# Kernel optimization log

Measured on AMD Instinct MI355X. Metric: run time of the kernel, lower is better.

Reference implementation:

```python
import jax, jax.numpy as jnp
import numpy as np

N = 100_000      # nodes
E = 1_600_000    # edges (avg degree 16)
D_IN, D_HID, D_OUT = 128, 64, 64
NEG_SLOPE = 0.2  # PyG GATConv default


def setup_inputs() -> dict:
    key = jax.random.key(0)
    ks = jax.random.split(key, 10)
    s = lambda k, shape: jax.random.normal(k, shape, jnp.float32) * 0.1
    return {
        "x": jax.random.normal(ks[0], (N, D_IN), jnp.float32),
        "edge_index": jax.random.randint(ks[1], (2, E), 0, N, dtype=jnp.int32),
        "W1": s(ks[2], (D_IN, D_HID)),
        "a_src1": s(ks[3], (D_HID,)),
        "a_dst1": s(ks[4], (D_HID,)),
        "b1": jnp.zeros((D_HID,), jnp.float32),
        "W2": s(ks[5], (D_HID, D_OUT)),
        "a_src2": s(ks[6], (D_OUT,)),
        "a_dst2": s(ks[7], (D_OUT,)),
        "b2": jnp.zeros((D_OUT,), jnp.float32),
    }


def gat_conv(x, src, dst, W, a_src, a_dst, b):
    """Single-head PyG-style GATConv (self-loops already appended to src/dst)."""
    n = x.shape[0]
    h = x @ W                                   # [N, D]
    # per-edge attention logits: leaky_relu(a_src . h_j + a_dst . h_i)
    logit = jax.nn.leaky_relu((h @ a_src)[src] + (h @ a_dst)[dst], NEG_SLOPE)
    # segment softmax over incoming edges of each dst node
    m = jax.ops.segment_max(logit, dst, num_segments=n)
    e = jnp.exp(logit - m[dst])
    denom = jax.ops.segment_sum(e, dst, num_segments=n)
    alpha = e / (denom[dst] + 1e-16)            # [E]
    out = jax.ops.segment_sum(alpha[:, None] * h[src], dst, num_segments=n)
    return out + b


def reference(x, edge_index, W1, a_src1, a_dst1, b1, W2, a_src2, a_dst2, b2):
    n = x.shape[0]
    loops = jnp.arange(n, dtype=edge_index.dtype)  # add_self_loops=True default
    src = jnp.concatenate([edge_index[0], loops])
    dst = jnp.concatenate([edge_index[1], loops])
    h = gat_conv(x, src, dst, W1, a_src1, a_dst1, b1)
    embedding = jax.nn.relu(h)   # dropout = identity (inference semantics)
    out = gat_conv(embedding, src, dst, W2, a_src2, a_dst2, b2)
    return (embedding, out)
```

## Files before the change

### kernel.cpp

```cpp
#include <hip/hip_runtime.h>
#include <hip/hip_bf16.h>

#define DHID 64
#define SUBSH 9
#define SUBSZ (1 << SUBSH)
#define PCAP 16384
#define EB 4096
typedef __attribute__((ext_vector_type(8))) short short8;
typedef __attribute__((ext_vector_type(4))) float f32x4;

static __device__ __forceinline__ short tobf(float f) {
  __hip_bfloat16 h = __float2bfloat16(f);
  return *reinterpret_cast<short*>(&h);
}

__global__ void k_bucket(const int* __restrict__ src, const int* __restrict__ dst,
                         int* __restrict__ bkt, int* __restrict__ bcnt,
                         int E, int nsb, int cap) {
  __shared__ int lcnt[256];
  __shared__ int lbase[256];
  int tid = threadIdx.x;
  int c0 = blockIdx.x * EB;
  if (c0 >= E) return;
  for (int i = tid; i < nsb; i += 256) lcnt[i] = 0;
  __syncthreads();
  int wloc[16], uloc[16];
  #pragma unroll
  for (int k = 0; k < 16; k++) {
    int i = c0 + tid + k * 256;
    if (i < E) {
      int d = dst[i];
      int w = d >> SUBSH;
      wloc[k] = w;
      uloc[k] = (src[i] << SUBSH) | (d & (SUBSZ - 1));
      atomicAdd(&lcnt[w], 1);
    } else wloc[k] = -1;
  }
  __syncthreads();
  for (int i = tid; i < nsb; i += 256) lbase[i] = atomicAdd(&bcnt[i], lcnt[i]);
  __syncthreads();
  for (int i = tid; i < nsb; i += 256) lcnt[i] = 0;
  __syncthreads();
  #pragma unroll
  for (int k = 0; k < 16; k++) {
    int w = wloc[k];
    if (w >= 0) {
      int r = atomicAdd(&lcnt[w], 1);
      bkt[(size_t)w * cap + lbase[w] + r] = uloc[k];
    }
  }
}

__global__ void k_count(const int* __restrict__ bkt, const int* __restrict__ bcnt,
                        int* __restrict__ roff, int N, int cap) {
  __shared__ int h[SUBSZ];
  int sb = blockIdx.x, tid = threadIdx.x;
  for (int j = tid; j < SUBSZ; j += 256) h[j] = 1;
  __syncthreads();
  int n = bcnt[sb];
  const int* b = bkt + (size_t)sb * cap;
  for (int i = tid; i < n; i += 256) atomicAdd(&h[b[i] & (SUBSZ - 1)], 1);
  __syncthreads();
  int d0 = sb << SUBSH, d1 = min(N, d0 + SUBSZ);
  for (int j = tid; j < d1 - d0; j += 256) roff[d0 + j] = h[j];
}

__global__ void k_scan_block(int* __restrict__ buf, int n, int* __restrict__ bsum) {
  __shared__ int lds[256];
  int tid = threadIdx.x;
  int base = blockIdx.x * 1024 + tid * 4;
  int a0 = (base + 0) < n ? buf[base + 0] : 0;
  int a1 = (base + 1) < n ? buf[base + 1] : 0;
  int a2 = (base + 2) < n ? buf[base + 2] : 0;
  int a3 = (base + 3) < n ? buf[base + 3] : 0;
  int s = a0 + a1 + a2 + a3;
  lds[tid] = s; __syncthreads();
  for (int off = 1; off < 256; off <<= 1) {
    int t = (tid >= off) ? lds[tid - off] : 0;
    __syncthreads();
    lds[tid] += t;
    __syncthreads();
  }
  int excl = lds[tid] - s;
  if ((base + 0) < n) buf[base + 0] = excl; excl += a0;
  if ((base + 1) < n) buf[base + 1] = excl; excl += a1;
  if ((base + 2) < n) buf[base + 2] = excl; excl += a2;
  if ((base + 3) < n) buf[base + 3] = excl;
  if (tid == 255) bsum[blockIdx.x] = lds[255];
}

__global__ void k_scan_mid(int* __restrict__ bsum, int nb) {
  int lane = threadIdx.x;
  int v0 = (lane < nb) ? bsum[lane] : 0;
  #pragma unroll
  for (int off = 1; off < 64; off <<= 1) { int t = __shfl_up(v0, off, 64); if (lane >= off) v0 += t; }
  int v1 = (64 + lane) < nb ? bsum[64 + lane] : 0;
  #pragma unroll
  for (int off = 1; off < 64; off <<= 1) { int t = __shfl_up(v1, off, 64); if (lane >= off) v1 += t; }
  v1 += __shfl(v0, 63, 64);
  if (lane < nb) bsum[lane] = v0;
  if ((64 + lane) < nb) bsum[64 + lane] = v1;
}

__global__ void k_scan_add(int* __restrict__ buf, int n, const int* __restrict__ bsum, int nb) {
  int i = blockIdx.x * blockDim.x + threadIdx.x;
  if (i < n) { int c = i >> 10; if (c > 0) buf[i] += bsum[c - 1]; }
  if (i == 0) buf[n] = bsum[nb - 1];
}

__global__ void k_place(const int* __restrict__ bkt, const int* __restrict__ bcnt,
                        const int* __restrict__ roff, int* __restrict__ csr,
                        int N, int cap) {
  __shared__ int roff_l[SUBSZ + 1];
  __shared__ int lcnt[SUBSZ];
  __shared__ int stage[PCAP];
  int sb = blockIdx.x, tid = threadIdx.x;
  int d0 = sb << SUBSH;
  int d1 = min(N, d0 + SUBSZ);
  int nn = d1 - d0;
  for (int j = tid; j <= nn; j += 256) roff_l[j] = roff[d0 + j];
  for (int j = tid; j < SUBSZ; j += 256) lcnt[j] = 0;
  __syncthreads();
  int base = roff_l[0];
  int span = roff_l[nn] - base;
  int nE = bcnt[sb];
  const int* b = bkt + (size_t)sb * cap;
  if (span <= PCAP) {
    for (int d = tid; d < nn; d += 256) stage[roff_l[d] - base] = (d0 + d) << 7;
    for (int i = tid; i < nE; i += 256) {
      int u = b[i];
      int dl = u & (SUBSZ - 1);
      int rk = 1 + atomicAdd(&lcnt[dl], 1);
      stage[roff_l[dl] - base + rk] = (u >> SUBSH) << 7;
    }
    __syncthreads();
    for (int j = tid; j < span; j += 256) csr[base + j] = stage[j];
  } else {
    for (int d = tid; d < nn; d += 256) csr[roff_l[d]] = (d0 + d) << 7;
    for (int i = tid; i < nE; i += 256) {
      int u = b[i];
      int dl = u & (SUBSZ - 1);
      int rk = 1 + atomicAdd(&lcnt[dl], 1);
      csr[roff_l[dl] + rk] = (u >> SUBSH) << 7;
    }
  }
}

__global__ void k_prep(const float* __restrict__ W, short* __restrict__ wt, int K) {
  int stride = gridDim.x * blockDim.x;
  for (int e = blockIdx.x * blockDim.x + threadIdx.x; e < 64 * K; e += stride) {
    int k = e >> 6, c = e & 63;
    wt[c * K + (k ^ ((c & 7) << 3))] = tobf(W[e]);
  }
}

template<int K, int AF32>
__launch_bounds__(256)
__global__ void k_mgemm(const float* __restrict__ xf, const short* __restrict__ xb,
                        const short* __restrict__ wt,
                        const float* __restrict__ a_s, const float* __restrict__ a_d,
                        short* __restrict__ hb, float* __restrict__ asb,
                        float* __restrict__ adb, int N) {
  constexpr int ASZ = 64 * K * 2;
  __shared__ __align__(16) short lds[(AF32 ? 1 : 2) * 64 * K];
  int tid = threadIdx.x;
  int n0 = blockIdx.x * 64;

  if (AF32) {
    const char* gb = (const char*)wt;
    #pragma unroll
    for (int j = 0; j < ASZ / 4096; j++) {
      int d = j * 4096 + tid * 16;
      __builtin_amdgcn_global_load_lds(
          (__attribute__((address_space(1))) const void*)(gb + d),
          (__attribute__((address_space(3))) void*)((char*)lds + d), 16, 0, 0);
    }
  } else {
    const char* ga = (const char*)xb + (size_t)n0 * (K * 2);
    const char* gb = (const char*)wt;
    #pragma unroll
    for (int j = 0; j < (2 * ASZ) / 4096; j++) {
      int d = j * 4096 + tid * 16;
      const char* src = (d < ASZ) ? (ga + d) : (gb + (d - ASZ));
      __builtin_amdgcn_global_load_lds(
          (__attribute__((address_space(1))) const void*)src,
          (__attribute__((address_space(3))) void*)((char*)lds + d), 16, 0, 0);
    }
  }
  __syncthreads();

  int l = tid & 63, w = tid >> 6;
  int c = l & 15, g = l >> 4;
  const short* A = lds;
  const short* B = AF32 ? lds : lds + 64 * K;
  f32x4 acc[4];
  #pragma unroll
  for (int t = 0; t < 4; t++) acc[t] = (f32x4){0.f, 0.f, 0.f, 0.f};

  int arow = 16 * w + c;
  short8 afr[K / 32];
  if (AF32) {
    int row = n0 + arow;
    const float* xr = xf + (size_t)row * 128;
    bool okr = row < N;
    #pragma unroll
    for (int s = 0; s < K / 32; s++) {
      int ke = s * 32 + g * 8;
      float4 u0 = make_float4(0.f, 0.f, 0.f, 0.f), u1 = u0;
      if (okr) { u0 = *(const float4*)(xr + ke); u1 = *(const float4*)(xr + ke + 4); }
      short8 af;
      af[0] = tobf(u0.x); af[1] = tobf(u0.y); af[2] = tobf(u0.z); af[3] = tobf(u0.w);
      af[4] = tobf(u1.x); af[5] = tobf(u1.y); af[6] = tobf(u1.z); af[7] = tobf(u1.w);
      afr[s] = af;
    }
  }

  #pragma unroll
  for (int s = 0; s < K / 32; s++) {
    int ke = s * 32 + g * 8;
    short8 af;
    if (AF32) af = afr[s];
    else      af = *(const short8*)(A + arow * K + (ke ^ ((arow & 7) << 3)));
    #pragma unroll
    for (int t = 0; t < 4; t++) {
      int bcol = 16 * t + c;
      short8 bf = *(const short8*)(B + bcol * K + (ke ^ ((bcol & 7) << 3)));
      acc[t] = __builtin_amdgcn_mfma_f32_16x16x32_bf16(af, bf, acc[t], 0, 0, 0);
    }
  }

  float av_s[4], av_d[4];
  #pragma unroll
  for (int t = 0; t < 4; t++) { av_s[t] = a_s[16 * t + c]; av_d[t] = a_d[16 * t + c]; }
  #pragma unroll
  for (int q = 0; q < 4; q++) {
    int row = n0 + 16 * w + g * 4 + q;
    bool ok = row < N;
    float rs = 0.f, rd = 0.f;
    #pragma unroll
    for (int t = 0; t < 4; t++) {
      float v = acc[t][q];
      if (ok) hb[(size_t)row * 64 + 16 * t + c] = tobf(v);
      rs += v * av_s[t]; rd += v * av_d[t];
    }
    #pragma unroll
    for (int off = 1; off < 16; off <<= 1) {
      rs += __shfl_xor(rs, off, 64);
      rd += __shfl_xor(rd, off, 64);
    }
    if (ok && c == 0) { asb[row] = rs; adb[row] = rd; }
  }
}

__global__ void k_agg(const int* __restrict__ roff, const int* __restrict__ csr,
                      const float* __restrict__ asb, const float* __restrict__ adb,
                      const short* __restrict__ hb, const float* __restrict__ b,
                      float* __restrict__ out, short* __restrict__ outb,
                      int N, int relu) {
  const char* hbase = (const char*)hb;
  int lane = threadIdx.x & 63;
  int colb = (lane & 15) * 8;
  int L = lane & 15;
  int wid = blockIdx.x * (blockDim.x >> 6) + (threadIdx.x >> 6);
  int nw = gridDim.x * (blockDim.x >> 6);
  float4 bv4 = ((const float4*)b)[L];
  for (int n = wid; n < N; n += nw) {
    int r0 = roff[n], r1 = roff[n + 1];
    float adn = adb[n];
    float a0 = 0.f, a1 = 0.f, a2 = 0.f, a3 = 0.f, denl = 0.f;
    for (int base = r0; base < r1; base += 64) {
      int cnt = min(64, r1 - base);
      int s128 = 0; float e = 0.f;
      if (lane < cnt) {
        s128 = csr[base + lane];
        float l = asb[s128 >> 7] + adn;
        l = fmaxf(l, 0.2f * l);
        e = __expf(l);
      }
      denl += e;
      int cntUp = (cnt + 3) & ~3;
      int addrv = (lane >> 4) << 2;
      #pragma unroll 2
      for (int j = 0; j < cntUp; j += 4) {
        int sofs = __builtin_amdgcn_ds_bpermute(addrv, s128);
        int ewi  = __builtin_amdgcn_ds_bpermute(addrv, (int)__float_as_uint(e));
        addrv += 16;
        float ew = __uint_as_float((unsigned)ewi);
        uint2 u = *(const uint2*)(hbase + (unsigned)(sofs + colb));
        a0 = fmaf(__uint_as_float(u.x << 16), ew, a0);
        a1 = fmaf(__uint_as_float(u.x & 0xFFFF0000u), ew, a1);
        a2 = fmaf(__uint_as_float(u.y << 16), ew, a2);
        a3 = fmaf(__uint_as_float(u.y & 0xFFFF0000u), ew, a3);
      }
    }
    #pragma unroll
    for (int off = 16; off <= 32; off <<= 1) {
      a0 += __shfl_xor(a0, off, 64); a1 += __shfl_xor(a1, off, 64);
      a2 += __shfl_xor(a2, off, 64); a3 += __shfl_xor(a3, off, 64);
    }
    float den = denl;
    #pragma unroll
    for (int off = 32; off; off >>= 1) den += __shfl_xor(den, off, 64);
    float inv = 1.f / (den + 1e-16f);
    if (lane < 16) {
      float4 o;
      o.x = fmaf(a0, inv, bv4.x); o.y = fmaf(a1, inv, bv4.y);
      o.z = fmaf(a2, inv, bv4.z); o.w = fmaf(a3, inv, bv4.w);
      if (relu) {
        o.x = fmaxf(o.x, 0.f); o.y = fmaxf(o.y, 0.f);
        o.z = fmaxf(o.z, 0.f); o.w = fmaxf(o.w, 0.f);
      }
      ((float4*)(out + (size_t)n * DHID))[L] = o;
      if (outb) {
        short4 ob = make_short4(tobf(o.x), tobf(o.y), tobf(o.z), tobf(o.w));
        ((short4*)(outb + (size_t)n * DHID))[L ^ ((n & 7) << 1)] = ob;
      }
    }
  }
}

extern "C" void kernel_launch(void* const* d_in, const int* in_sizes, int n_in,
                              void* d_out, int out_size, void* d_ws, size_t ws_size,
                              hipStream_t stream) {
  const float* x   = (const float*)d_in[0];
  const int*   ei  = (const int*)d_in[1];
  const float* W1  = (const float*)d_in[2];
  const float* as1 = (const float*)d_in[3];
  const float* ad1 = (const float*)d_in[4];
  const float* b1  = (const float*)d_in[5];
  const float* W2  = (const float*)d_in[6];
  const float* as2 = (const float*)d_in[7];
  const float* ad2 = (const float*)d_in[8];
  const float* b2  = (const float*)d_in[9];

  int N = in_sizes[0] / 128;
  int E = in_sizes[1] / 2;
  const int* srcp = ei;
  const int* dstp = ei + E;

  float* emb  = (float*)d_out;
  float* out2 = emb + (size_t)N * DHID;

  char* w = (char*)d_ws;
  auto alloc = [&](size_t bytes) { char* p = w; w += (bytes + 255) & ~(size_t)255; return p; };
  int NR = ((N + 63) / 64) * 64;
  int* roff = (int*)alloc((size_t)(N + 1) * 4);
  int* csr  = (int*)alloc((size_t)(E + N) * 4);
  int* bsum = (int*)alloc(2048);
  char* scr0 = alloc((size_t)NR * 128 * 2);
  short* hb = (short*)alloc((size_t)NR * 64 * 2);
  float* asb = (float*)alloc((size_t)N * 4);
  float* adb = (float*)alloc((size_t)N * 4);
  short* wt1 = (short*)alloc(64 * 128 * 2);
  short* wt2 = (short*)alloc(64 * 64 * 2);
  short* eb = (short*)scr0;
  int* bkt  = (int*)scr0;
  int* bcnt = (int*)hb;

  int nsb = (N + SUBSZ - 1) >> SUBSH;
  int cap = E / nsb + 4096;

  int nb = (N + 1023) / 1024;
  int NBLK = (N + 63) / 64;

  hipMemsetAsync(bcnt, 0, (size_t)nsb * 4, stream);
  k_bucket<<<(E + EB - 1) / EB, 256, 0, stream>>>(srcp, dstp, bkt, bcnt, E, nsb, cap);
  k_count<<<nsb, 256, 0, stream>>>(bkt, bcnt, roff, N, cap);
  k_scan_block<<<nb, 256, 0, stream>>>(roff, N, bsum);
  k_scan_mid<<<1, 64, 0, stream>>>(bsum, nb);
  k_scan_add<<<(N + 255) / 256, 256, 0, stream>>>(roff, N, bsum, nb);
  k_place<<<nsb, 256, 0, stream>>>(bkt, bcnt, roff, csr, N, cap);

  k_prep<<<32, 256, 0, stream>>>(W1, wt1, 128);
  k_prep<<<32, 256, 0, stream>>>(W2, wt2, 64);

  k_mgemm<128, 1><<<NBLK, 256, 0, stream>>>(x, nullptr, wt1, as1, ad1, hb, asb, adb, N);
  k_agg<<<2048, 256, 0, stream>>>(roff, csr, asb, adb, hb, b1, emb, eb, N, 1);
  k_mgemm<64, 0><<<NBLK, 256, 0, stream>>>(nullptr, eb, wt2, as2, ad2, hb, asb, adb, N);
  k_agg<<<2048, 256, 0, stream>>>(roff, csr, asb, adb, hb, b2, out2, (short*)nullptr, N, 0);
}
```

Before: 184.0 us.

## Fuse edge bucketing with layer-1 GEMM and fold weight prep into GEMMs

Merges the edge-bucketing kernel and the first-layer GEMM into one launch: the low block indices bucket edges and the remaining blocks compute x@W1 and the attention projections. The separate weight-prep kernels are removed, and each GEMM block now converts and swizzles W to bf16 into LDS itself. Bucketing keeps per-edge LDS ranks from the first pass, so the second atomic pass is dropped, and the edge chunk per block is halved. The bcnt buffer gets its own allocation because hb is now written concurrently, and the aggregation inner loop unroll goes from 2 to 4. Together this cuts kernel launches and lets the bucket and GEMM work overlap, at the cost of redundant per-block weight conversion.

```diff
diff --git a/kernel.cpp b/kernel.cpp
--- a/kernel.cpp
+++ b/kernel.cpp
@@ -5,7 +5,7 @@
 #define SUBSH 9
 #define SUBSZ (1 << SUBSH)
 #define PCAP 16384
-#define EB 4096
+#define EB 2048
 typedef __attribute__((ext_vector_type(8))) short short8;
 typedef __attribute__((ext_vector_type(4))) float f32x4;
 
@@ -14,40 +14,166 @@
   return *reinterpret_cast<short*>(&h);
 }
 
-__global__ void k_bucket(const int* __restrict__ src, const int* __restrict__ dst,
-                         int* __restrict__ bkt, int* __restrict__ bcnt,
-                         int E, int nsb, int cap) {
+__global__ __launch_bounds__(256)
+void k_fusedA(const int* __restrict__ src, const int* __restrict__ dst,
+              int* __restrict__ bkt, int* __restrict__ bcnt,
+              int E, int nsb, int cap, int nbkt,
+              const float* __restrict__ xf, const float* __restrict__ W1,
+              const float* __restrict__ a_s, const float* __restrict__ a_d,
+              short* __restrict__ hb, float* __restrict__ asb,
+              float* __restrict__ adb, int N) {
   __shared__ int lcnt[256];
   __shared__ int lbase[256];
+  __shared__ __align__(16) short ldsB[64 * 128];
   int tid = threadIdx.x;
-  int c0 = blockIdx.x * EB;
-  if (c0 >= E) return;
-  for (int i = tid; i < nsb; i += 256) lcnt[i] = 0;
-  __syncthreads();
-  int wloc[16], uloc[16];
-  #pragma unroll
-  for (int k = 0; k < 16; k++) {
-    int i = c0 + tid + k * 256;
-    if (i < E) {
-      int d = dst[i];
-      int w = d >> SUBSH;
-      wloc[k] = w;
-      uloc[k] = (src[i] << SUBSH) | (d & (SUBSZ - 1));
-      atomicAdd(&lcnt[w], 1);
-    } else wloc[k] = -1;
-  }
-  __syncthreads();
-  for (int i = tid; i < nsb; i += 256) lbase[i] = atomicAdd(&bcnt[i], lcnt[i]);
-  __syncthreads();
-  for (int i = tid; i < nsb; i += 256) lcnt[i] = 0;
-  __syncthreads();
-  #pragma unroll
-  for (int k = 0; k < 16; k++) {
-    int w = wloc[k];
-    if (w >= 0) {
-      int r = atomicAdd(&lcnt[w], 1);
-      bkt[(size_t)w * cap + lbase[w] + r] = uloc[k];
-    }
+  if (blockIdx.x < nbkt) {
+    int c0 = blockIdx.x * EB;
+    for (int i = tid; i < nsb; i += 256) lcnt[i] = 0;
+    __syncthreads();
+    int wloc[8], uloc[8], rloc[8];
+    #pragma unroll
+    for (int k = 0; k < 8; k++) {
+      int i = c0 + tid + k * 256;
+      if (i < E) {
+        int d = dst[i];
+        int w = d >> SUBSH;
+        wloc[k] = w;
+        uloc[k] = (src[i] << SUBSH) | (d & (SUBSZ - 1));
+        rloc[k] = atomicAdd(&lcnt[w], 1);
+      } else wloc[k] = -1;
+    }
+    __syncthreads();
+    for (int i = tid; i < nsb; i += 256) lbase[i] = atomicAdd(&bcnt[i], lcnt[i]);
+    __syncthreads();
+    #pragma unroll
+    for (int k = 0; k < 8; k++) {
+      int w = wloc[k];
+      if (w >= 0) bkt[(size_t)w * cap + lbase[w] + rloc[k]] = uloc[k];
+    }
+    return;
+  }
+  int n0 = (blockIdx.x - nbkt) * 64;
+  for (int e = tid; e < 128 * 64; e += 256) {
+    int k = e >> 6, c = e & 63;
+    ldsB[c * 128 + (k ^ ((c & 7) << 3))] = tobf(W1[e]);
+  }
+  __syncthreads();
+
+  int l = tid & 63, w = tid >> 6;
+  int c = l & 15, g = l >> 4;
+  f32x4 acc[4];
+  #pragma unroll
+  for (int t = 0; t < 4; t++) acc[t] = (f32x4){0.f, 0.f, 0.f, 0.f};
+
+  int arow = 16 * w + c;
+  int row0 = n0 + arow;
+  const float* xr = xf + (size_t)row0 * 128;
+  bool okr = row0 < N;
+  short8 afr[4];
+  #pragma unroll
+  for (int s = 0; s < 4; s++) {
+    int ke = s * 32 + g * 8;
+    float4 u0 = make_float4(0.f, 0.f, 0.f, 0.f), u1 = u0;
+    if (okr) { u0 = *(const float4*)(xr + ke); u1 = *(const float4*)(xr + ke + 4); }
+    short8 af;
+    af[0] = tobf(u0.x); af[1] = tobf(u0.y); af[2] = tobf(u0.z); af[3] = tobf(u0.w);
+    af[4] = tobf(u1.x); af[5] = tobf(u1.y); af[6] = tobf(u1.z); af[7] = tobf(u1.w);
+    afr[s] = af;
+  }
+  #pragma unroll
+  for (int s = 0; s < 4; s++) {
+    int ke = s * 32 + g * 8;
+    #pragma unroll
+    for (int t = 0; t < 4; t++) {
+      int bcol = 16 * t + c;
+      short8 bf = *(const short8*)(ldsB + bcol * 128 + (ke ^ ((bcol & 7) << 3)));
+      acc[t] = __builtin_amdgcn_mfma_f32_16x16x32_bf16(afr[s], bf, acc[t], 0, 0, 0);
+    }
+  }
+  float av_s[4], av_d[4];
+  #pragma unroll
+  for (int t = 0; t < 4; t++) { av_s[t] = a_s[16 * t + c]; av_d[t] = a_d[16 * t + c]; }
+  #pragma unroll
+  for (int q = 0; q < 4; q++) {
+    int row = n0 + 16 * w + g * 4 + q;
+    bool ok = row < N;
+    float rs = 0.f, rd = 0.f;
+    #pragma unroll
+    for (int t = 0; t < 4; t++) {
+      float v = acc[t][q];
+      if (ok) hb[(size_t)row * 64 + 16 * t + c] = tobf(v);
+      rs += v * av_s[t]; rd += v * av_d[t];
+    }
+    #pragma unroll
+    for (int off = 1; off < 16; off <<= 1) {
+      rs += __shfl_xor(rs, off, 64);
+      rd += __shfl_xor(rd, off, 64);
+    }
+    if (ok && c == 0) { asb[row] = rs; adb[row] = rd; }
+  }
+}
+
+__global__ __launch_bounds__(256)
+void k_mgemm2(const short* __restrict__ eb, const float* __restrict__ W2,
+              const float* __restrict__ a_s, const float* __restrict__ a_d,
+              short* __restrict__ hb, float* __restrict__ asb,
+              float* __restrict__ adb, int N) {
+  __shared__ __align__(16) short lds[64 * 64 * 2];
+  int tid = threadIdx.x;
+  int n0 = blockIdx.x * 64;
+  const char* ga = (const char*)eb + (size_t)n0 * 128;
+  #pragma unroll
+  for (int j = 0; j < 2; j++) {
+    int d = j * 4096 + tid * 16;
+    __builtin_amdgcn_global_load_lds(
+        (__attribute__((address_space(1))) const void*)(ga + d),
+        (__attribute__((address_space(3))) void*)((char*)lds + d), 16, 0, 0);
+  }
+  short* B = lds + 64 * 64;
+  for (int e = tid; e < 64 * 64; e += 256) {
+    int k = e >> 6, c = e & 63;
+    B[c * 64 + (k ^ ((c & 7) << 3))] = tobf(W2[e]);
+  }
+  __syncthreads();
+
+  int l = tid & 63, w = tid >> 6;
+  int c = l & 15, g = l >> 4;
+  const short* A = lds;
+  f32x4 acc[4];
+  #pragma unroll
+  for (int t = 0; t < 4; t++) acc[t] = (f32x4){0.f, 0.f, 0.f, 0.f};
+  int arow = 16 * w + c;
+  #pragma unroll
+  for (int s = 0; s < 2; s++) {
+    int ke = s * 32 + g * 8;
+    short8 af = *(const short8*)(A + arow * 64 + (ke ^ ((arow & 7) << 3)));
+    #pragma unroll
+    for (int t = 0; t < 4; t++) {
+      int bcol = 16 * t + c;
+      short8 bf = *(const short8*)(B + bcol * 64 + (ke ^ ((bcol & 7) << 3)));
+      acc[t] = __builtin_amdgcn_mfma_f32_16x16x32_bf16(af, bf, acc[t], 0, 0, 0);
+    }
+  }
+  float av_s[4], av_d[4];
+  #pragma unroll
+  for (int t = 0; t < 4; t++) { av_s[t] = a_s[16 * t + c]; av_d[t] = a_d[16 * t + c]; }
+  #pragma unroll
+  for (int q = 0; q < 4; q++) {
+    int row = n0 + 16 * w + g * 4 + q;
+    bool ok = row < N;
+    float rs = 0.f, rd = 0.f;
+    #pragma unroll
+    for (int t = 0; t < 4; t++) {
+      float v = acc[t][q];
+      if (ok) hb[(size_t)row * 64 + 16 * t + c] = tobf(v);
+      rs += v * av_s[t]; rd += v * av_d[t];
+    }
+    #pragma unroll
+    for (int off = 1; off < 16; off <<= 1) {
+      rs += __shfl_xor(rs, off, 64);
+      rd += __shfl_xor(rd, off, 64);
+    }
+    if (ok && c == 0) { asb[row] = rs; adb[row] = rd; }
   }
 }
 
@@ -143,112 +269,6 @@
       int rk = 1 + atomicAdd(&lcnt[dl], 1);
       csr[roff_l[dl] + rk] = (u >> SUBSH) << 7;
     }
-  }
-}
-
-__global__ void k_prep(const float* __restrict__ W, short* __restrict__ wt, int K) {
-  int stride = gridDim.x * blockDim.x;
-  for (int e = blockIdx.x * blockDim.x + threadIdx.x; e < 64 * K; e += stride) {
-    int k = e >> 6, c = e & 63;
-    wt[c * K + (k ^ ((c & 7) << 3))] = tobf(W[e]);
-  }
-}
-
-template<int K, int AF32>
-__launch_bounds__(256)
-__global__ void k_mgemm(const float* __restrict__ xf, const short* __restrict__ xb,
-                        const short* __restrict__ wt,
-                        const float* __restrict__ a_s, const float* __restrict__ a_d,
-                        short* __restrict__ hb, float* __restrict__ asb,
-                        float* __restrict__ adb, int N) {
-  constexpr int ASZ = 64 * K * 2;
-  __shared__ __align__(16) short lds[(AF32 ? 1 : 2) * 64 * K];
-  int tid = threadIdx.x;
-  int n0 = blockIdx.x * 64;
-
-  if (AF32) {
-    const char* gb = (const char*)wt;
-    #pragma unroll
-    for (int j = 0; j < ASZ / 4096; j++) {
-      int d = j * 4096 + tid * 16;
-      __builtin_amdgcn_global_load_lds(
-          (__attribute__((address_space(1))) const void*)(gb + d),
-          (__attribute__((address_space(3))) void*)((char*)lds + d), 16, 0, 0);
-    }
-  } else {
-    const char* ga = (const char*)xb + (size_t)n0 * (K * 2);
-    const char* gb = (const char*)wt;
-    #pragma unroll
-    for (int j = 0; j < (2 * ASZ) / 4096; j++) {
-      int d = j * 4096 + tid * 16;
-      const char* src = (d < ASZ) ? (ga + d) : (gb + (d - ASZ));
-      __builtin_amdgcn_global_load_lds(
-          (__attribute__((address_space(1))) const void*)src,
-          (__attribute__((address_space(3))) void*)((char*)lds + d), 16, 0, 0);
-    }
-  }
-  __syncthreads();
-
-  int l = tid & 63, w = tid >> 6;
-  int c = l & 15, g = l >> 4;
-  const short* A = lds;
-  const short* B = AF32 ? lds : lds + 64 * K;
-  f32x4 acc[4];
-  #pragma unroll
-  for (int t = 0; t < 4; t++) acc[t] = (f32x4){0.f, 0.f, 0.f, 0.f};
-
-  int arow = 16 * w + c;
-  short8 afr[K / 32];
-  if (AF32) {
-    int row = n0 + arow;
-    const float* xr = xf + (size_t)row * 128;
-    bool okr = row < N;
-    #pragma unroll
-    for (int s = 0; s < K / 32; s++) {
-      int ke = s * 32 + g * 8;
-      float4 u0 = make_float4(0.f, 0.f, 0.f, 0.f), u1 = u0;
-      if (okr) { u0 = *(const float4*)(xr + ke); u1 = *(const float4*)(xr + ke + 4); }
-      short8 af;
-      af[0] = tobf(u0.x); af[1] = tobf(u0.y); af[2] = tobf(u0.z); af[3] = tobf(u0.w);
-      af[4] = tobf(u1.x); af[5] = tobf(u1.y); af[6] = tobf(u1.z); af[7] = tobf(u1.w);
-      afr[s] = af;
-    }
-  }
-
-  #pragma unroll
-  for (int s = 0; s < K / 32; s++) {
-    int ke = s * 32 + g * 8;
-    short8 af;
-    if (AF32) af = afr[s];
-    else      af = *(const short8*)(A + arow * K + (ke ^ ((arow & 7) << 3)));
-    #pragma unroll
-    for (int t = 0; t < 4; t++) {
-      int bcol = 16 * t + c;
-      short8 bf = *(const short8*)(B + bcol * K + (ke ^ ((bcol & 7) << 3)));
-      acc[t] = __builtin_amdgcn_mfma_f32_16x16x32_bf16(af, bf, acc[t], 0, 0, 0);
-    }
-  }
-
-  float av_s[4], av_d[4];
-  #pragma unroll
-  for (int t = 0; t < 4; t++) { av_s[t] = a_s[16 * t + c]; av_d[t] = a_d[16 * t + c]; }
-  #pragma unroll
-  for (int q = 0; q < 4; q++) {
-    int row = n0 + 16 * w + g * 4 + q;
-    bool ok = row < N;
-    float rs = 0.f, rd = 0.f;
-    #pragma unroll
-    for (int t = 0; t < 4; t++) {
-      float v = acc[t][q];
-      if (ok) hb[(size_t)row * 64 + 16 * t + c] = tobf(v);
-      rs += v * av_s[t]; rd += v * av_d[t];
-    }
-    #pragma unroll
-    for (int off = 1; off < 16; off <<= 1) {
-      rs += __shfl_xor(rs, off, 64);
-      rd += __shfl_xor(rd, off, 64);
-    }
-    if (ok && c == 0) { asb[row] = rs; adb[row] = rd; }
   }
 }
 
@@ -280,7 +300,7 @@
       denl += e;
       int cntUp = (cnt + 3) & ~3;
       int addrv = (lane >> 4) << 2;
-      #pragma unroll 2
+      #pragma unroll 4
       for (int j = 0; j < cntUp; j += 4) {
         int sofs = __builtin_amdgcn_ds_bpermute(addrv, s128);
         int ewi  = __builtin_amdgcn_ds_bpermute(addrv, (int)__float_as_uint(e));
@@ -347,35 +367,31 @@
   int* roff = (int*)alloc((size_t)(N + 1) * 4);
   int* csr  = (int*)alloc((size_t)(E + N) * 4);
   int* bsum = (int*)alloc(2048);
+  int* bcnt = (int*)alloc(1024);
   char* scr0 = alloc((size_t)NR * 128 * 2);
   short* hb = (short*)alloc((size_t)NR * 64 * 2);
   float* asb = (float*)alloc((size_t)N * 4);
   float* adb = (float*)alloc((size_t)N * 4);
-  short* wt1 = (short*)alloc(64 * 128 * 2);
-  short* wt2 = (short*)alloc(64 * 64 * 2);
   short* eb = (short*)scr0;
   int* bkt  = (int*)scr0;
-  int* bcnt = (int*)hb;
 
   int nsb = (N + SUBSZ - 1) >> SUBSH;
   int cap = E / nsb + 4096;
 
   int nb = (N + 1023) / 1024;
   int NBLK = (N + 63) / 64;
+  int nbkt = (E + EB - 1) / EB;
 
   hipMemsetAsync(bcnt, 0, (size_t)nsb * 4, stream);
-  k_bucket<<<(E + EB - 1) / EB, 256, 0, stream>>>(srcp, dstp, bkt, bcnt, E, nsb, cap);
+  k_fusedA<<<nbkt + NBLK, 256, 0, stream>>>(srcp, dstp, bkt, bcnt, E, nsb, cap, nbkt,
+                                            x, W1, as1, ad1, hb, asb, adb, N);
   k_count<<<nsb, 256, 0, stream>>>(bkt, bcnt, roff, N, cap);
   k_scan_block<<<nb, 256, 0, stream>>>(roff, N, bsum);
   k_scan_mid<<<1, 64, 0, stream>>>(bsum, nb);
   k_scan_add<<<(N + 255) / 256, 256, 0, stream>>>(roff, N, bsum, nb);
   k_place<<<nsb, 256, 0, stream>>>(bkt, bcnt, roff, csr, N, cap);
 
-  k_prep<<<32, 256, 0, stream>>>(W1, wt1, 128);
-  k_prep<<<32, 256, 0, stream>>>(W2, wt2, 64);
-
-  k_mgemm<128, 1><<<NBLK, 256, 0, stream>>>(x, nullptr, wt1, as1, ad1, hb, asb, adb, N);
   k_agg<<<2048, 256, 0, stream>>>(roff, csr, asb, adb, hb, b1, emb, eb, N, 1);
-  k_mgemm<64, 0><<<NBLK, 256, 0, stream>>>(nullptr, eb, wt2, as2, ad2, hb, asb, adb, N);
+  k_mgemm2<<<NBLK, 256, 0, stream>>>(eb, W2, as2, ad2, hb, asb, adb, N);
   k_agg<<<2048, 256, 0, stream>>>(roff, csr, asb, adb, hb, b2, out2, (short*)nullptr, N, 0);
 }
```

After: 180.5 us. No clear change (-1.9%).
